# Performance work log

Hardware: AMD Instinct MI355X
Metric: run time of the kernel (lower is better)

## Reference

```python
import jax, jax.numpy as jnp
import numpy as np

NUM_FEAT = 512
NUM_HEAD = 8
DEPTH = NUM_FEAT // NUM_HEAD
B, S = 2, 4096


def setup_inputs() -> dict:
    key = jax.random.key(0)
    ks = jax.random.split(key, 12)
    sc = 1.0 / np.sqrt(NUM_FEAT)
    inp = {
        "q": jax.random.normal(ks[0], (B, S, NUM_FEAT), jnp.float32),
        "k": jax.random.normal(ks[1], (B, S, NUM_FEAT), jnp.float32),
        "v": jax.random.normal(ks[2], (B, S, NUM_FEAT), jnp.float32),
        # causal mask: 1 where attention is disallowed (upper triangle), additive style
        "mask": jnp.triu(jnp.ones((S, S), jnp.float32), k=1)[None, None, :, :],
        "wq": jax.random.normal(ks[3], (NUM_FEAT, NUM_FEAT), jnp.float32) * sc,
        "bq": jnp.zeros((NUM_FEAT,), jnp.float32),
        "wk": jax.random.normal(ks[4], (NUM_FEAT, NUM_FEAT), jnp.float32) * sc,
        "bk": jnp.zeros((NUM_FEAT,), jnp.float32),
        "wv": jax.random.normal(ks[5], (NUM_FEAT, NUM_FEAT), jnp.float32) * sc,
        "bv": jnp.zeros((NUM_FEAT,), jnp.float32),
        "wo": jax.random.normal(ks[6], (NUM_FEAT, NUM_FEAT), jnp.float32) * sc,
        "bo": jnp.zeros((NUM_FEAT,), jnp.float32),
    }
    return inp


def _split_heads(x):
    b, s, _ = x.shape
    return x.reshape(b, s, NUM_HEAD, DEPTH).transpose(0, 2, 1, 3)  # [B,H,S,D]


def reference(q, k, v, mask, wq, bq, wk, bk, wv, bv, wo, bo):
    qh = _split_heads(q @ wq + bq)
    kh = _split_heads(k @ wk + bk)
    vh = _split_heads(v @ wv + bv)
    # scaled dot-product attention with materialized [B,H,S,S] scores
    logits = jnp.einsum("bhqd,bhkd->bhqk", qh, kh) / jnp.sqrt(jnp.float32(DEPTH))
    logits = logits + mask * (-1e9)
    weights = jax.nn.softmax(logits, axis=-1)
    attn = jnp.einsum("bhqk,bhkd->bhqd", weights, vh)
    concat = attn.transpose(0, 2, 1, 3).reshape(q.shape[0], -1, NUM_FEAT)
    return concat @ wo + bo
```

## Files before the change

kernel.cpp:

```cpp
#include <hip/hip_runtime.h>
#include <hip/hip_bf16.h>
#include <stdint.h>

#define NB 2
#define NS 4096
#define NF 512
#define NH 8
#define ND 64
#define NM (NB * NS)

typedef __attribute__((ext_vector_type(8))) short bf16x8;
typedef __attribute__((ext_vector_type(4))) float f32x4;
typedef __attribute__((ext_vector_type(16))) float f32x16;

static __device__ __forceinline__ unsigned short f2bf(float f) {
    union { float f; uint32_t u; } x; x.f = f;
    uint32_t u = x.u;
    u += 0x7FFFu + ((u >> 16) & 1u);
    return (unsigned short)(u >> 16);
}

static __device__ __forceinline__ void load_lds16(const void* g, void* l) {
    __builtin_amdgcn_global_load_lds(
        (const __attribute__((address_space(1))) void*)g,
        (__attribute__((address_space(3))) void*)l,
        16, 0, 0);
}

__global__ void convert_all(const float* __restrict__ q, const float* __restrict__ k,
                            const float* __restrict__ v,
                            unsigned short* __restrict__ qb, unsigned short* __restrict__ kb,
                            unsigned short* __restrict__ vb,
                            const float* __restrict__ wq, const float* __restrict__ wk,
                            const float* __restrict__ wv, const float* __restrict__ wo,
                            unsigned short* __restrict__ o0, unsigned short* __restrict__ o1,
                            unsigned short* __restrict__ o2, unsigned short* __restrict__ o3) {
    int i0 = blockIdx.x * blockDim.x + threadIdx.x;
    int stride = gridDim.x * blockDim.x;
    const int n4 = (NB * NS * NF) / 4;
    for (int i = i0; i < n4; i += stride) {
        float4 a = ((const float4*)q)[i];
        float4 b = ((const float4*)k)[i];
        float4 c = ((const float4*)v)[i];
        ushort4 oa, ob, oc;
        oa.x = f2bf(a.x); oa.y = f2bf(a.y); oa.z = f2bf(a.z); oa.w = f2bf(a.w);
        ob.x = f2bf(b.x); ob.y = f2bf(b.y); ob.z = f2bf(b.z); ob.w = f2bf(b.w);
        oc.x = f2bf(c.x); oc.y = f2bf(c.y); oc.z = f2bf(c.z); oc.w = f2bf(c.w);
        ((ushort4*)qb)[i] = oa;
        ((ushort4*)kb)[i] = ob;
        ((ushort4*)vb)[i] = oc;
    }
    for (int i = i0; i < 4 * NF * NF; i += stride) {
        int w = i >> 18;
        int off = i & (NF * NF - 1);
        int r = off >> 9;
        int c = off & (NF - 1);
        const float* src = (w == 0) ? wq : (w == 1) ? wk : (w == 2) ? wv : wo;
        unsigned short* dst = (w == 0) ? o0 : (w == 1) ? o1 : (w == 2) ? o2 : o3;
        dst[c * NF + r] = f2bf(src[off]);
    }
}

__launch_bounds__(256, 2)
__global__ void proj_qkv(const unsigned short* __restrict__ Aq,
                         const unsigned short* __restrict__ Ak,
                         const unsigned short* __restrict__ Av,
                         const unsigned short* __restrict__ WqT,
                         const unsigned short* __restrict__ WkT,
                         const unsigned short* __restrict__ WvT,
                         const float* __restrict__ bq, const float* __restrict__ bk,
                         const float* __restrict__ bv,
                         unsigned short* __restrict__ Qh, unsigned short* __restrict__ Kh,
                         unsigned short* __restrict__ VTs) {
    __shared__ char smem[65536];

    const int mode = blockIdx.z;
    const unsigned short* A  = (mode == 0) ? Aq : (mode == 1) ? Ak : Av;
    const unsigned short* WT = (mode == 0) ? WqT : (mode == 1) ? WkT : WvT;
    const float* bias        = (mode == 0) ? bq : (mode == 1) ? bk : bv;

    const int t = threadIdx.x;
    const int wid = t >> 6;
    const int lane = t & 63;
    const int l15 = lane & 15;
    const int lhi = lane >> 4;
    const int m0 = blockIdx.x * 128;
    const int n0 = blockIdx.y * 128;
    const int wm = (wid >> 1) * 64;
    const int wn = (wid & 1) * 64;

    const int srow = t >> 3;
    const int scol = ((t & 7) * 16) ^ ((srow & 7) << 4);

    const f32x4 zero4 = {0.f, 0.f, 0.f, 0.f};
    f32x4 acc[4][4];
#pragma unroll
    for (int i = 0; i < 4; ++i)
#pragma unroll
        for (int j = 0; j < 4; ++j) acc[i][j] = zero4;

    auto STAGE = [&](int buf, int k0) {
        char* As = smem + buf * 32768;
        char* Bs = As + 16384;
#pragma unroll
        for (int i = 0; i < 4; ++i) {
            const char* sa = (const char*)A + ((size_t)(m0 + i * 32 + srow) * NF + k0) * 2 + scol;
            load_lds16(sa, As + i * 4096 + wid * 1024);
            const char* sb = (const char*)WT + ((size_t)(n0 + i * 32 + srow) * NF + k0) * 2 + scol;
            load_lds16(sb, Bs + i * 4096 + wid * 1024);
        }
    };

    STAGE(0, 0);
    int cur = 0;
    for (int kt = 0; kt < 8; ++kt) {
        if (kt < 7) {
            STAGE(cur ^ 1, (kt + 1) * 64);
            asm volatile("s_waitcnt vmcnt(8)" ::: "memory");
        } else {
            asm volatile("s_waitcnt vmcnt(0)" ::: "memory");
        }
        __builtin_amdgcn_s_barrier();
        __builtin_amdgcn_sched_barrier(0);

        const char* As = smem + cur * 32768;
        const char* Bs = As + 16384;
#pragma unroll
        for (int ks = 0; ks < 2; ++ks) {
            bf16x8 af[4], bfr[4];
#pragma unroll
            for (int i = 0; i < 4; ++i) {
                int ra = wm + i * 16 + l15;
                int ca = (ks * 64 + lhi * 16) ^ ((ra & 7) << 4);
                af[i] = *(const bf16x8*)(As + ra * 128 + ca);
                int rb = wn + i * 16 + l15;
                int cb = (ks * 64 + lhi * 16) ^ ((rb & 7) << 4);
                bfr[i] = *(const bf16x8*)(Bs + rb * 128 + cb);
            }
#pragma unroll
            for (int mi = 0; mi < 4; ++mi)
#pragma unroll
                for (int ni = 0; ni < 4; ++ni)
                    acc[mi][ni] = __builtin_amdgcn_mfma_f32_16x16x32_bf16(af[mi], bfr[ni], acc[mi][ni], 0, 0, 0);
        }
        __builtin_amdgcn_sched_barrier(0);
        __builtin_amdgcn_s_barrier();
        cur ^= 1;
    }

#pragma unroll
    for (int ni = 0; ni < 4; ++ni) {
        int col = n0 + wn + ni * 16 + l15;
        float bv2 = bias[col];
#pragma unroll
        for (int mi = 0; mi < 4; ++mi) {
#pragma unroll
            for (int r = 0; r < 4; ++r) {
                int row = m0 + wm + mi * 16 + lhi * 4 + r;
                float val = acc[mi][ni][r] + bv2;
                int b = row >> 12, s = row & (NS - 1);
                int hh = col >> 6, d = col & (ND - 1);
                if (mode == 0) {
                    val *= 0.125f;
                    Qh[((size_t)(b * NH + hh) * NS + s) * ND + d] = f2bf(val);
                } else if (mode == 1) {
                    Kh[((size_t)(b * NH + hh) * NS + s) * ND + d] = f2bf(val);
                } else {
                    VTs[((size_t)(b * NH + hh) * ND + d) * NS + s] = f2bf(val);
                }
            }
        }
    }
}

__launch_bounds__(256, 2)
__global__ void proj_o(const unsigned short* __restrict__ A,
                       const unsigned short* __restrict__ WT,
                       const float* __restrict__ bias,
                       float* __restrict__ Out) {
    __shared__ char smem[49152];

    const int t = threadIdx.x;
    const int wid = t >> 6;
    const int lane = t & 63;
    const int l15 = lane & 15;
    const int lhi = lane >> 4;
    const int m0 = blockIdx.x * 64;
    const int n0 = blockIdx.y * 128;
    const int wm = (wid >> 1) * 32;
    const int wn = (wid & 1) * 64;

    const int srow = t >> 3;
    const int scol = ((t & 7) * 16) ^ ((srow & 7) << 4);

    const f32x4 zero4 = {0.f, 0.f, 0.f, 0.f};
    f32x4 acc[2][4];
#pragma unroll
    for (int i = 0; i < 2; ++i)
#pragma unroll
        for (int j = 0; j < 4; ++j) acc[i][j] = zero4;

    auto STAGE = [&](int buf, int k0) {
        char* As = smem + buf * 24576;
        char* Bs = As + 8192;
#pragma unroll
        for (int i = 0; i < 2; ++i) {
            const char* sa = (const char*)A + ((size_t)(m0 + i * 32 + srow) * NF + k0) * 2 + scol;
            load_lds16(sa, As + i * 4096 + wid * 1024);
        }
#pragma unroll
        for (int i = 0; i < 4; ++i) {
            const char* sb = (const char*)WT + ((size_t)(n0 + i * 32 + srow) * NF + k0) * 2 + scol;
            load_lds16(sb, Bs + i * 4096 + wid * 1024);
        }
    };

    STAGE(0, 0);
    int cur = 0;
    for (int kt = 0; kt < 8; ++kt) {
        if (kt < 7) {
            STAGE(cur ^ 1, (kt + 1) * 64);
            asm volatile("s_waitcnt vmcnt(6)" ::: "memory");
        } else {
            asm volatile("s_waitcnt vmcnt(0)" ::: "memory");
        }
        __builtin_amdgcn_s_barrier();
        __builtin_amdgcn_sched_barrier(0);

        const char* As = smem + cur * 24576;
        const char* Bs = As + 8192;
#pragma unroll
        for (int ks = 0; ks < 2; ++ks) {
            bf16x8 af[2], bfr[4];
#pragma unroll
            for (int i = 0; i < 2; ++i) {
                int ra = wm + i * 16 + l15;
                int ca = (ks * 64 + lhi * 16) ^ ((ra & 7) << 4);
                af[i] = *(const bf16x8*)(As + ra * 128 + ca);
            }
#pragma unroll
            for (int i = 0; i < 4; ++i) {
                int rb = wn + i * 16 + l15;
                int cb = (ks * 64 + lhi * 16) ^ ((rb & 7) << 4);
                bfr[i] = *(const bf16x8*)(Bs + rb * 128 + cb);
            }
#pragma unroll
            for (int mi = 0; mi < 2; ++mi)
#pragma unroll
                for (int ni = 0; ni < 4; ++ni)
                    acc[mi][ni] = __builtin_amdgcn_mfma_f32_16x16x32_bf16(af[mi], bfr[ni], acc[mi][ni], 0, 0, 0);
        }
        __builtin_amdgcn_sched_barrier(0);
        __builtin_amdgcn_s_barrier();
        cur ^= 1;
    }

#pragma unroll
    for (int ni = 0; ni < 4; ++ni) {
        int col = n0 + wn + ni * 16 + l15;
        float bv2 = bias[col];
#pragma unroll
        for (int mi = 0; mi < 2; ++mi)
#pragma unroll
            for (int r = 0; r < 4; ++r) {
                int row = m0 + wm + mi * 16 + lhi * 4 + r;
                Out[(size_t)row * NF + col] = acc[mi][ni][r] + bv2;
            }
    }
}

__launch_bounds__(64, 2)
__global__ void attn_fused(const unsigned short* __restrict__ Qh,
                           const unsigned short* __restrict__ Kh,
                           const unsigned short* __restrict__ VT,
                           unsigned short* __restrict__ Cc) {
    const int lane = threadIdx.x;
    const int l31 = lane & 31;
    const int h = lane >> 5;
    const int k = blockIdx.x;
    const int bh = k & 15;
    const int g = 127 - (k >> 4);
    const int b = bh >> 3, hh = bh & 7;
    const size_t bhs = (size_t)b * NH + hh;
    const char* Qp = (const char*)(Qh + bhs * NS * ND);
    const char* Kp = (const char*)(Kh + bhs * NS * ND);
    const char* Vp = (const char*)(VT + bhs * (size_t)ND * NS);

    const int qrow = g * 32 + l31;
    bf16x8 qf[4];
#pragma unroll
    for (int kc = 0; kc < 4; ++kc)
        qf[kc] = *(const bf16x8*)(Qp + (size_t)qrow * 128 + kc * 32 + h * 16);

    f32x16 o[2];
#pragma unroll
    for (int r = 0; r < 16; ++r) { o[0][r] = 0.f; o[1][r] = 0.f; }
    float m_run = -1e30f, l_run = 0.f;

    const int nkv = (g >> 1) + 1;

    auto LOADK = [&](int t, bf16x8* kf) {
        const char* base = Kp + (size_t)t * 64 * 128;
#pragma unroll
        for (int kvi = 0; kvi < 2; ++kvi)
#pragma unroll
            for (int kc = 0; kc < 4; ++kc)
                kf[kvi * 4 + kc] = *(const bf16x8*)(base + (kvi * 32 + l31) * 128 + kc * 32 + h * 16);
    };
    auto LOADV = [&](int t, bf16x8* vf) {
        const char* base = Vp + (size_t)t * 128;
#pragma unroll
        for (int di = 0; di < 2; ++di)
#pragma unroll
            for (int ck = 0; ck < 4; ++ck)
                vf[di * 4 + ck] = *(const bf16x8*)(base + (size_t)(di * 32 + l31) * (NS * 2) + ck * 32 + h * 16);
    };

    auto TILE = [&](int t, const bf16x8* kf, const bf16x8* vf) {
        f32x16 sT[2];
#pragma unroll
        for (int r = 0; r < 16; ++r) { sT[0][r] = 0.f; sT[1][r] = 0.f; }
#pragma unroll
        for (int kvi = 0; kvi < 2; ++kvi)
#pragma unroll
            for (int kc = 0; kc < 4; ++kc)
                sT[kvi] = __builtin_amdgcn_mfma_f32_32x32x16_bf16(kf[kvi * 4 + kc], qf[kc], sT[kvi], 0, 0, 0);

        if (t == nkv - 1) {
#pragma unroll
            for (int kvi = 0; kvi < 2; ++kvi)
#pragma unroll
                for (int r = 0; r < 16; ++r) {
                    int kv = t * 64 + kvi * 32 + (r & 3) + ((r >> 2) << 3) + h * 4;
                    if (kv > qrow) sT[kvi][r] = -1e30f;
                }
        }

        float pm = -1e30f;
#pragma unroll
        for (int kvi = 0; kvi < 2; ++kvi)
#pragma unroll
            for (int r = 0; r < 16; ++r) pm = fmaxf(pm, sT[kvi][r]);
        pm = fmaxf(pm, __shfl_xor(pm, 32));

        if (__ballot(pm > m_run + 8.0f) != 0ull) {
            float mnew = fmaxf(m_run, pm);
            float sc = __expf(m_run - mnew);
            m_run = mnew;
            l_run *= sc;
#pragma unroll
            for (int di = 0; di < 2; ++di)
#pragma unroll
                for (int r = 0; r < 16; ++r) o[di][r] *= sc;
        }
        float rs = 0.f;
#pragma unroll
        for (int kvi = 0; kvi < 2; ++kvi)
#pragma unroll
            for (int r = 0; r < 16; ++r) {
                float p = __expf(sT[kvi][r] - m_run);
                sT[kvi][r] = p;
                rs += p;
            }
        rs += __shfl_xor(rs, 32);
        l_run += rs;

        unsigned int w[2][8];
#pragma unroll
        for (int kvi = 0; kvi < 2; ++kvi)
#pragma unroll
            for (int i = 0; i < 8; ++i)
                w[kvi][i] = (unsigned int)f2bf(sT[kvi][2 * i]) |
                            ((unsigned int)f2bf(sT[kvi][2 * i + 1]) << 16);

        union FB { unsigned int u[4]; bf16x8 v; };
        bf16x8 pf[4];
#pragma unroll
        for (int ck = 0; ck < 4; ++ck) {
            const int kvi = ck >> 1, pb = (ck & 1) * 4;
            unsigned int aSrc = h ? w[kvi][pb + 0] : w[kvi][pb + 2];
            unsigned int bSrc = h ? w[kvi][pb + 1] : w[kvi][pb + 3];
            unsigned int sA = (unsigned int)__shfl_xor((int)aSrc, 32);
            unsigned int sB = (unsigned int)__shfl_xor((int)bSrc, 32);
            FB f;
            f.u[0] = (h == 0) ? w[kvi][pb + 0] : sA;
            f.u[1] = (h == 0) ? w[kvi][pb + 1] : sB;
            f.u[2] = (h == 0) ? sA : w[kvi][pb + 2];
            f.u[3] = (h == 0) ? sB : w[kvi][pb + 3];
            pf[ck] = f.v;
        }

#pragma unroll
        for (int di = 0; di < 2; ++di)
#pragma unroll
            for (int ck = 0; ck < 4; ++ck)
                o[di] = __builtin_amdgcn_mfma_f32_32x32x16_bf16(vf[di * 4 + ck], pf[ck], o[di], 0, 0, 0);
    };

    bf16x8 kA[8], kB[8], vv[8];
    LOADK(0, kA);
    int t = 0;
    while (true) {
        LOADV(t, vv);
        if (t + 1 < nkv) LOADK(t + 1, kB);
        TILE(t, kA, vv);
        if (++t >= nkv) break;
        LOADV(t, vv);
        if (t + 1 < nkv) LOADK(t + 1, kA);
        TILE(t, kB, vv);
        if (++t >= nkv) break;
    }

    float inv = 1.0f / l_run;
    size_t obase = ((size_t)b * NS + qrow) * NF + hh * ND;
#pragma unroll
    for (int di = 0; di < 2; ++di)
#pragma unroll
        for (int tq = 0; tq < 4; ++tq) {
            ushort4 pk;
            pk.x = f2bf(o[di][4 * tq + 0] * inv);
            pk.y = f2bf(o[di][4 * tq + 1] * inv);
            pk.z = f2bf(o[di][4 * tq + 2] * inv);
            pk.w = f2bf(o[di][4 * tq + 3] * inv);
            *(ushort4*)(Cc + obase + di * 32 + tq * 8 + h * 4) = pk;
        }
}

extern "C" void kernel_launch(void* const* d_in, const int* in_sizes, int n_in,
                              void* d_out, int out_size, void* d_ws, size_t ws_size,
                              hipStream_t stream) {
    const float* q = (const float*)d_in[0];
    const float* k = (const float*)d_in[1];
    const float* v = (const float*)d_in[2];
    const float* wq = (const float*)d_in[4];
    const float* bq = (const float*)d_in[5];
    const float* wk = (const float*)d_in[6];
    const float* bk = (const float*)d_in[7];
    const float* wv = (const float*)d_in[8];
    const float* bv = (const float*)d_in[9];
    const float* wo = (const float*)d_in[10];
    const float* bo = (const float*)d_in[11];

    const size_t MB = 1u << 20;
    char* ws = (char*)d_ws;
    unsigned short* qb  = (unsigned short*)(ws);
    unsigned short* kb  = (unsigned short*)(ws + 8 * MB);
    unsigned short* vb  = (unsigned short*)(ws + 16 * MB);
    unsigned short* wqT = (unsigned short*)(ws + 24 * MB);
    unsigned short* wkT = (unsigned short*)(ws + 24 * MB + 512 * 1024);
    unsigned short* wvT = (unsigned short*)(ws + 25 * MB);
    unsigned short* woT = (unsigned short*)(ws + 25 * MB + 512 * 1024);
    unsigned short* Qh  = (unsigned short*)(ws + 26 * MB);
    unsigned short* Kh  = (unsigned short*)(ws + 34 * MB);
    unsigned short* VTs = (unsigned short*)(ws + 42 * MB);

    convert_all<<<dim3(2048), dim3(256), 0, stream>>>(q, k, v, qb, kb, vb,
                                                      wq, wk, wv, wo, wqT, wkT, wvT, woT);

    proj_qkv<<<dim3(NM / 128, NF / 128, 3), dim3(256), 0, stream>>>(
        qb, kb, vb, wqT, wkT, wvT, bq, bk, bv, Qh, Kh, VTs);

    attn_fused<<<dim3(2048), dim3(64), 0, stream>>>(Qh, Kh, VTs, qb );

    proj_o<<<dim3(NM / 64, NF / 128), dim3(256), 0, stream>>>(qb, woT, bo, (float*)d_out);
}
```

Before: 334.3 us.

## Split causal attention KV range across two blocks and merge with combine kernel

Each query tile's KV loop is split into two halves processed by separate blocks. Each block writes an unnormalized bf16 partial output plus its running max and sum, and a new combine kernel rescales and merges them into the concat buffer. This is meant to raise parallelism and shorten the longest causal tiles. The softmax switches to exp2, with log2(e) folded into the Q scale, and uses the hardware packed bf16 convert. The weight transpose now reads strided and writes contiguously. Costs are an extra kernel launch, extra partial-result traffic, and a bf16 rounding of the partial outputs before merging.

```diff
diff --git a/kernel.cpp b/kernel.cpp
--- a/kernel.cpp
+++ b/kernel.cpp
@@ -8,6 +8,7 @@
 #define NH 8
 #define ND 64
 #define NM (NB * NS)
+#define NROW (NB * NH * NS)
 
 typedef __attribute__((ext_vector_type(8))) short bf16x8;
 typedef __attribute__((ext_vector_type(4))) float f32x4;
@@ -18,6 +19,15 @@
     uint32_t u = x.u;
     u += 0x7FFFu + ((u >> 16) & 1u);
     return (unsigned short)(u >> 16);
+}
+static __device__ __forceinline__ float bf2f(unsigned short u) {
+    union { uint32_t u; float f; } x; x.u = ((uint32_t)u) << 16;
+    return x.f;
+}
+static __device__ __forceinline__ unsigned int cvtpk(float lo, float hi) {
+    unsigned int r;
+    asm("v_cvt_pk_bf16_f32 %0, %1, %2" : "=v"(r) : "v"(lo), "v"(hi));
+    return r;
 }
 
 static __device__ __forceinline__ void load_lds16(const void* g, void* l) {
@@ -50,14 +60,14 @@
         ((ushort4*)kb)[i] = ob;
         ((ushort4*)vb)[i] = oc;
     }
-    for (int i = i0; i < 4 * NF * NF; i += stride) {
-        int w = i >> 18;
-        int off = i & (NF * NF - 1);
-        int r = off >> 9;
-        int c = off & (NF - 1);
+    for (int j = i0; j < 4 * NF * NF; j += stride) {
+        int w = j >> 18;
+        int off = j & (NF * NF - 1);
+        int n = off >> 9;
+        int kq = off & (NF - 1);
         const float* src = (w == 0) ? wq : (w == 1) ? wk : (w == 2) ? wv : wo;
         unsigned short* dst = (w == 0) ? o0 : (w == 1) ? o1 : (w == 2) ? o2 : o3;
-        dst[c * NF + r] = f2bf(src[off]);
+        dst[off] = f2bf(src[kq * NF + n]);
     }
 }
 
@@ -161,7 +171,7 @@
                 int b = row >> 12, s = row & (NS - 1);
                 int hh = col >> 6, d = col & (ND - 1);
                 if (mode == 0) {
-                    val *= 0.125f;
+                    val *= 0.1803368801111244f;
                     Qh[((size_t)(b * NH + hh) * NS + s) * ND + d] = f2bf(val);
                 } else if (mode == 1) {
                     Kh[((size_t)(b * NH + hh) * NS + s) * ND + d] = f2bf(val);
@@ -269,17 +279,21 @@
     }
 }
 
-__launch_bounds__(64, 2)
+__launch_bounds__(64, 4)
 __global__ void attn_fused(const unsigned short* __restrict__ Qh,
                            const unsigned short* __restrict__ Kh,
                            const unsigned short* __restrict__ VT,
-                           unsigned short* __restrict__ Cc) {
+                           unsigned short* __restrict__ Op,
+                           float* __restrict__ Mp,
+                           float* __restrict__ Lp) {
     const int lane = threadIdx.x;
     const int l31 = lane & 31;
     const int h = lane >> 5;
     const int k = blockIdx.x;
-    const int bh = k & 15;
-    const int g = 127 - (k >> 4);
+    const int pr = k & 1;
+    const int kk = k >> 1;
+    const int bh = kk & 15;
+    const int g = 127 - (kk >> 4);
     const int b = bh >> 3, hh = bh & 7;
     const size_t bhs = (size_t)b * NH + hh;
     const char* Qp = (const char*)(Qh + bhs * NS * ND);
@@ -298,6 +312,9 @@
     float m_run = -1e30f, l_run = 0.f;
 
     const int nkv = (g >> 1) + 1;
+    const int hsp = (nkv + 1) >> 1;
+    const int tbeg = pr ? hsp : 0;
+    const int tend = pr ? nkv : hsp;
 
     auto LOADK = [&](int t, bf16x8* kf) {
         const char* base = Kp + (size_t)t * 64 * 128;
@@ -343,9 +360,9 @@
             for (int r = 0; r < 16; ++r) pm = fmaxf(pm, sT[kvi][r]);
         pm = fmaxf(pm, __shfl_xor(pm, 32));
 
-        if (__ballot(pm > m_run + 8.0f) != 0ull) {
+        if (__ballot(pm > m_run + 11.5f) != 0ull) {
             float mnew = fmaxf(m_run, pm);
-            float sc = __expf(m_run - mnew);
+            float sc = __builtin_amdgcn_exp2f(m_run - mnew);
             m_run = mnew;
             l_run *= sc;
 #pragma unroll
@@ -358,7 +375,7 @@
         for (int kvi = 0; kvi < 2; ++kvi)
 #pragma unroll
             for (int r = 0; r < 16; ++r) {
-                float p = __expf(sT[kvi][r] - m_run);
+                float p = __builtin_amdgcn_exp2f(sT[kvi][r] - m_run);
                 sT[kvi][r] = p;
                 rs += p;
             }
@@ -370,8 +387,7 @@
         for (int kvi = 0; kvi < 2; ++kvi)
 #pragma unroll
             for (int i = 0; i < 8; ++i)
-                w[kvi][i] = (unsigned int)f2bf(sT[kvi][2 * i]) |
-                            ((unsigned int)f2bf(sT[kvi][2 * i + 1]) << 16);
+                w[kvi][i] = cvtpk(sT[kvi][2 * i], sT[kvi][2 * i + 1]);
 
         union FB { unsigned int u[4]; bf16x8 v; };
         bf16x8 pf[4];
@@ -397,33 +413,61 @@
                 o[di] = __builtin_amdgcn_mfma_f32_32x32x16_bf16(vf[di * 4 + ck], pf[ck], o[di], 0, 0, 0);
     };
 
-    bf16x8 kA[8], kB[8], vv[8];
-    LOADK(0, kA);
-    int t = 0;
-    while (true) {
-        LOADV(t, vv);
-        if (t + 1 < nkv) LOADK(t + 1, kB);
-        TILE(t, kA, vv);
-        if (++t >= nkv) break;
-        LOADV(t, vv);
-        if (t + 1 < nkv) LOADK(t + 1, kA);
-        TILE(t, kB, vv);
-        if (++t >= nkv) break;
-    }
-
-    float inv = 1.0f / l_run;
-    size_t obase = ((size_t)b * NS + qrow) * NF + hh * ND;
+    if (tbeg < tend) {
+        bf16x8 kA[8], kB[8], vv[8];
+        LOADK(tbeg, kA);
+        int t = tbeg;
+        while (true) {
+            LOADV(t, vv);
+            if (t + 1 < tend) LOADK(t + 1, kB);
+            TILE(t, kA, vv);
+            if (++t >= tend) break;
+            LOADV(t, vv);
+            if (t + 1 < tend) LOADK(t + 1, kA);
+            TILE(t, kB, vv);
+            if (++t >= tend) break;
+        }
+    }
+
+    const int prow = bh * NS + qrow;
+    size_t pb = ((size_t)pr * NROW + prow) * 64;
 #pragma unroll
     for (int di = 0; di < 2; ++di)
 #pragma unroll
         for (int tq = 0; tq < 4; ++tq) {
-            ushort4 pk;
-            pk.x = f2bf(o[di][4 * tq + 0] * inv);
-            pk.y = f2bf(o[di][4 * tq + 1] * inv);
-            pk.z = f2bf(o[di][4 * tq + 2] * inv);
-            pk.w = f2bf(o[di][4 * tq + 3] * inv);
-            *(ushort4*)(Cc + obase + di * 32 + tq * 8 + h * 4) = pk;
-        }
+            uint2 pk;
+            pk.x = cvtpk(o[di][4 * tq + 0], o[di][4 * tq + 1]);
+            pk.y = cvtpk(o[di][4 * tq + 2], o[di][4 * tq + 3]);
+            *(uint2*)(Op + pb + di * 32 + tq * 8 + h * 4) = pk;
+        }
+    if (h == 0) {
+        Mp[pr * NROW + prow] = m_run;
+        Lp[pr * NROW + prow] = l_run;
+    }
+}
+
+__global__ void attn_combine(const unsigned short* __restrict__ Op,
+                             const float* __restrict__ Mp, const float* __restrict__ Lp,
+                             unsigned short* __restrict__ Cc) {
+    int i = blockIdx.x * blockDim.x + threadIdx.x;
+    int row = i >> 4;
+    int d4 = (i & 15) << 2;
+    float m0 = Mp[row], m1 = Mp[NROW + row];
+    float l0 = Lp[row], l1 = Lp[NROW + row];
+    float m = fmaxf(m0, m1);
+    float e0 = __builtin_amdgcn_exp2f(m0 - m);
+    float e1 = __builtin_amdgcn_exp2f(m1 - m);
+    float inv = 1.0f / (l0 * e0 + l1 * e1);
+    e0 *= inv; e1 *= inv;
+    ushort4 a = *(const ushort4*)(Op + (size_t)row * 64 + d4);
+    ushort4 c = *(const ushort4*)(Op + (size_t)NROW * 64 + (size_t)row * 64 + d4);
+    ushort4 r;
+    r.x = f2bf(bf2f(a.x) * e0 + bf2f(c.x) * e1);
+    r.y = f2bf(bf2f(a.y) * e0 + bf2f(c.y) * e1);
+    r.z = f2bf(bf2f(a.z) * e0 + bf2f(c.z) * e1);
+    r.w = f2bf(bf2f(a.w) * e0 + bf2f(c.w) * e1);
+    int bb = row >> 15, hh = (row >> 12) & 7, s = row & (NS - 1);
+    *(ushort4*)(Cc + ((size_t)(bb * NS + s) * NF) + hh * ND + d4) = r;
 }
 
 extern "C" void kernel_launch(void* const* d_in, const int* in_sizes, int n_in,
@@ -454,13 +498,19 @@
     unsigned short* Kh  = (unsigned short*)(ws + 34 * MB);
     unsigned short* VTs = (unsigned short*)(ws + 42 * MB);
 
+    unsigned short* Opart = kb;
+    float* Mpart = (float*)(ws + 24 * MB);
+    float* Lpart = (float*)(ws + 24 * MB + 512 * 1024);
+
     convert_all<<<dim3(2048), dim3(256), 0, stream>>>(q, k, v, qb, kb, vb,
                                                       wq, wk, wv, wo, wqT, wkT, wvT, woT);
 
     proj_qkv<<<dim3(NM / 128, NF / 128, 3), dim3(256), 0, stream>>>(
         qb, kb, vb, wqT, wkT, wvT, bq, bk, bv, Qh, Kh, VTs);
 
-    attn_fused<<<dim3(2048), dim3(64), 0, stream>>>(Qh, Kh, VTs, qb );
+    attn_fused<<<dim3(4096), dim3(64), 0, stream>>>(Qh, Kh, VTs, Opart, Mpart, Lpart);
+
+    attn_combine<<<dim3(NROW * 16 / 256), dim3(256), 0, stream>>>(Opart, Mpart, Lpart, qb);
 
     proj_o<<<dim3(NM / 64, NF / 128), dim3(256), 0, stream>>>(qb, woT, bo, (float*)d_out);
 }
```

Result: slower. 513.4 us (+53.6%).
